# Optimization experiments

Hardware: AMD Instinct MI355X
Metric: run time of the kernel (lower is better)

## Reference

```python
import jax, jax.numpy as jnp
import numpy as np
from jax import lax

DN = ('NCHW', 'OIHW', 'NCHW')
BETA = 0.25


def _conv(x, w, b, stride, pad):
    y = lax.conv_general_dilated(x, w, (stride, stride), [(pad, pad), (pad, pad)],
                                 dimension_numbers=DN)
    return y + b[None, :, None, None]


def _convT(x, w, b, stride, pad, opad):
    # torch ConvTranspose2d(w: [in,out,kh,kw]) == dilated conv with flipped, transposed kernel
    k = w.shape[2]
    wf = jnp.transpose(w, (1, 0, 2, 3))[:, :, ::-1, ::-1]
    lo = k - 1 - pad
    hi = k - 1 - pad + opad
    y = lax.conv_general_dilated(x, wf, (1, 1), [(lo, hi), (lo, hi)],
                                 lhs_dilation=(stride, stride), dimension_numbers=DN)
    return y + b[None, :, None, None]


def setup_inputs() -> dict:
    key = jax.random.key(0)
    ks = jax.random.split(key, 16)
    s = 0.05
    inp = {
        'x': jax.random.normal(ks[0], (64, 3, 125, 125), jnp.float32),
        'enc_w1': jax.random.normal(ks[1], (32, 3, 3, 3), jnp.float32) * s,
        'enc_b1': jnp.zeros((32,), jnp.float32),
        'enc_w2': jax.random.normal(ks[2], (64, 32, 3, 3), jnp.float32) * s,
        'enc_b2': jnp.zeros((64,), jnp.float32),
        'enc_w3': jax.random.normal(ks[3], (64, 64, 1, 1), jnp.float32) * s,
        'enc_b3': jnp.zeros((64,), jnp.float32),
        'codebook': jax.random.normal(ks[4], (512, 64), jnp.float32),
        'dec_w1': jax.random.normal(ks[5], (64, 64, 3, 3), jnp.float32) * s,  # torch [in,out,kh,kw]
        'dec_b1': jnp.zeros((64,), jnp.float32),
        'dec_w2': jax.random.normal(ks[6], (64, 32, 3, 3), jnp.float32) * s,
        'dec_b2': jnp.zeros((32,), jnp.float32),
        'dec_w3': jax.random.normal(ks[7], (32, 3, 2, 2), jnp.float32) * s,
        'dec_b3': jnp.zeros((3,), jnp.float32),
    }
    return inp


def reference(x, enc_w1, enc_b1, enc_w2, enc_b2, enc_w3, enc_b3, codebook,
              dec_w1, dec_b1, dec_w2, dec_b2, dec_w3, dec_b3):
    # Encoder
    z = jax.nn.relu(_conv(x, enc_w1, enc_b1, 2, 1))
    z = jax.nn.relu(_conv(z, enc_w2, enc_b2, 2, 1))
    z = _conv(z, enc_w3, enc_b3, 1, 0)  # [B, D, h, w]

    # VQ (training mode)
    zp = jnp.transpose(z, (0, 2, 3, 1))  # [B, h, w, D]
    flat = zp.reshape(-1, zp.shape[-1])  # [N, D]
    d = (jnp.sum(flat * flat, axis=1, keepdims=True)
         + jnp.sum(codebook * codebook, axis=1)
         - 2.0 * flat @ codebook.T)  # [N, K]
    idx = jnp.argmin(d, axis=1)
    q = codebook[idx].reshape(zp.shape)

    q_latent_loss = jnp.mean((q - lax.stop_gradient(zp)) ** 2)
    e_latent_loss = jnp.mean((zp - lax.stop_gradient(q)) ** 2)
    e_q_loss = q_latent_loss + BETA * e_latent_loss

    q_st = zp + lax.stop_gradient(q - zp)  # straight-through
    e = jnp.transpose(q_st, (0, 3, 1, 2))

    # Decoder
    h = jax.nn.relu(_convT(e, dec_w1, dec_b1, 2, 1, 1))
    h = jax.nn.relu(_convT(h, dec_w2, dec_b2, 2, 1, 1))
    x_recon = _convT(h, dec_w3, dec_b3, 1, 2, 0)

    recon_loss = jnp.sum((x_recon - x) ** 2)
    loss_sum = e_q_loss + recon_loss
    return (loss_sum, e_q_loss, recon_loss, x_recon)
```

## Files before the change

kernel.cpp:

```cpp
#include <hip/hip_runtime.h>

#define DEV __device__ __forceinline__
typedef unsigned short u16;
typedef __bf16 bf16x8 __attribute__((ext_vector_type(8)));
typedef float f32x4 __attribute__((ext_vector_type(4)));

DEV u16 f2bf(float f) {
  unsigned u = __float_as_uint(f);
  u += 0x7FFF + ((u >> 16) & 1);
  return (u16)(u >> 16);
}


__global__ __launch_bounds__(256) void k_prep(
    const float* __restrict__ ew1, const float* __restrict__ ew2,
    const float* __restrict__ ew3, const float* __restrict__ dw1,
    const float* __restrict__ dw2, const float* __restrict__ dw3,
    const float* __restrict__ cb,
    float* __restrict__ wc1p, float* __restrict__ wc3p,
    u16* __restrict__ w3f, float* __restrict__ c2,
    u16* __restrict__ w2f, u16* __restrict__ wt1f, u16* __restrict__ wt2f,
    u16* __restrict__ cbf) {
  int i = blockIdx.x * 256 + threadIdx.x;
  if (i < 864) {
    int cl = i & 7; int t = i >> 3; int tap = t % 9; t /= 9; int ci = t % 3; int cog = t / 3;
    wc1p[i] = ew1[((cog * 8 + cl) * 3 + ci) * 9 + tap];
  } else if (i < 4960) {
    int j = i - 864; int cl = j & 7; int t = j >> 3; int ci = t & 63; int cog = t >> 6;
    wc3p[j] = ew3[(cog * 8 + cl) * 64 + ci];
  } else if (i < 9056) {
    int j = i - 4960;
    int jj = j & 7; int lane = (j >> 3) & 63; int tp = (j >> 9) & 3; int hl = j >> 11;
    int kh = tp >> 1, kw = tp & 1;
    int ci = ((lane >> 4) << 3) + jj; int co = lane & 15;
    float wv = (co < 3) ? dw3[((ci * 3 + co) * 2 + kh) * 2 + kw] : 0.f;
    u16 hi = f2bf(wv);
    if (hl == 0) w3f[j] = hi;
    else         w3f[j] = f2bf(wv - __uint_as_float((unsigned)hi << 16));
  } else if (i < 9568) {
    int k = i - 9056;
    const float4* c4 = (const float4*)(cb + (k << 6));
    float s = 0.f;
    #pragma unroll
    for (int q = 0; q < 16; ++q) { float4 v = c4[q]; s += v.x*v.x + v.y*v.y + v.z*v.z + v.w*v.w; }
    c2[k] = s;
  } else if (i < 28000) {
    int j = i - 9568;
    int jj = j & 7; int lane = (j >> 3) & 63; int nf = (j >> 9) & 3; int kt = j >> 11;
    int kh = kt / 3, kw = kt % 3;
    int ci = ((lane >> 4) << 3) + jj; int co = (nf << 4) + (lane & 15);
    w2f[j] = f2bf(ew2[((co * 32 + ci) * 3 + kh) * 3 + kw]);
  } else if (i < 64864) {
    int j = i - 28000;
    int jj = j & 7; int lane = (j >> 3) & 63; int nf = (j >> 9) & 3; int s = (j >> 11) & 1; int kt = j >> 12;
    int kh = kt / 3, kw = kt % 3;
    int ci = (s << 5) + ((lane >> 4) << 3) + jj; int co = (nf << 4) + (lane & 15);
    wt1f[j] = f2bf(dw1[((ci * 64 + co) * 3 + kh) * 3 + kw]);
  } else if (i < 83296) {
    int j = i - 64864;
    int jj = j & 7; int lane = (j >> 3) & 63; int nf = (j >> 9) & 1; int s = (j >> 10) & 1; int kt = j >> 11;
    int kh = kt / 3, kw = kt % 3;
    int ci = (s << 5) + ((lane >> 4) << 3) + jj; int co = (nf << 4) + (lane & 15);
    wt2f[j] = f2bf(dw2[((ci * 32 + co) * 3 + kh) * 3 + kw]);
  } else if (i < 148832) {
    int j = i - 83296;
    int jj = j & 7; int lane = (j >> 3) & 63; int nt = (j >> 9) & 31; int ks = (j >> 14) & 1; int hl = j >> 15;
    int ci = (ks << 5) + ((lane >> 4) << 3) + jj;
    int code = (nt << 4) + (lane & 15);
    float v = cb[(code << 6) + ci];
    u16 hi = f2bf(v);
    cbf[j] = hl ? f2bf(v - __uint_as_float((unsigned)hi << 16)) : hi;
  }
}

__global__ __launch_bounds__(256) void k_pad(
    const float* __restrict__ x, float* __restrict__ xp) {
  int idx = blockIdx.x * 256 + threadIdx.x;
  int c4 = idx & 31;
  int r  = (idx >> 5) % 129;
  int cbp = (idx >> 5) / 129;
  int ih = r - 1;
  float4 v = make_float4(0.f, 0.f, 0.f, 0.f);
  if ((unsigned)ih < 125u) {
    const float* rp = x + (cbp * 125 + ih) * 125;
    int iw0 = c4 * 4 - 1;
    if (iw0 >= 0)        v.x = rp[iw0];
    if (iw0 + 1 < 125)   v.y = rp[iw0 + 1];
    if (iw0 + 2 < 125)   v.z = rp[iw0 + 2];
    if (iw0 + 3 < 125)   v.w = rp[iw0 + 3];
  }
  *(float4*)(xp + (cbp * 129 + r) * 128 + c4 * 4) = v;
}

__global__ __launch_bounds__(256) void k_conv1(
    const float* __restrict__ xp, const float* __restrict__ wp,
    const float* __restrict__ bias, u16* __restrict__ z1t) {
  __shared__ u16 st[256 * 34];
  int t = threadIdx.x;
  int slab = blockIdx.x & 15, b = blockIdx.x >> 4;
  int tx = t & 15, ty = (t >> 4) & 3, cg = t >> 6;
  int oh = slab * 4 + ty;
  int co0 = cg * 8;
  const float* wcg = wp + cg * 216;
  float acc[8][4];
  #pragma unroll
  for (int c = 0; c < 8; ++c) {
    float bv = bias[co0 + c];
    #pragma unroll
    for (int s = 0; s < 4; ++s) acc[c][s] = bv;
  }
  #pragma unroll
  for (int ci = 0; ci < 3; ++ci) {
    #pragma unroll
    for (int kh = 0; kh < 3; ++kh) {
      const float* rp = xp + ((b * 3 + ci) * 129 + (2 * oh + kh)) * 128 + 8 * tx;
      float4 qa = *(const float4*)rp;
      float4 qb = *(const float4*)(rp + 4);
      float v8 = rp[8];
      float v[9] = {qa.x, qa.y, qa.z, qa.w, qb.x, qb.y, qb.z, qb.w, v8};
      #pragma unroll
      for (int kw = 0; kw < 3; ++kw) {
        const float* wq = wcg + (ci * 9 + kh * 3 + kw) * 8;
        float4 wa = *(const float4*)wq;
        float4 wb = *(const float4*)(wq + 4);
        float w8[8] = {wa.x, wa.y, wa.z, wa.w, wb.x, wb.y, wb.z, wb.w};
        #pragma unroll
        for (int s = 0; s < 4; ++s) {
          float in = v[2 * s + kw];
          #pragma unroll
          for (int c = 0; c < 8; ++c) acc[c][s] = fmaf(in, w8[c], acc[c][s]);
        }
      }
    }
  }
  #pragma unroll
  for (int s = 0; s < 4; ++s) {
    bool wok = (tx * 4 + s) < 63;
    unsigned p0 = 0, p1 = 0, p2 = 0, p3 = 0;
    if (wok) {
      p0 = f2bf(fmaxf(acc[0][s], 0.f)) | ((unsigned)f2bf(fmaxf(acc[1][s], 0.f)) << 16);
      p1 = f2bf(fmaxf(acc[2][s], 0.f)) | ((unsigned)f2bf(fmaxf(acc[3][s], 0.f)) << 16);
      p2 = f2bf(fmaxf(acc[4][s], 0.f)) | ((unsigned)f2bf(fmaxf(acc[5][s], 0.f)) << 16);
      p3 = f2bf(fmaxf(acc[6][s], 0.f)) | ((unsigned)f2bf(fmaxf(acc[7][s], 0.f)) << 16);
    }
    int lpix = tx * 16 + ty * 4 + s;
    *(uint4*)&st[lpix * 34 + co0] = make_uint4(p0, p1, p2, p3);
  }
  __syncthreads();
  {
    int p = t;
    int ow = (p >> 4) * 4 + (p & 3);
    int ohl = (p >> 2) & 3;
    int oho = slab * 4 + ohl;
    if (oho < 63) {
      const u16* lp = &st[p * 34];
      uint4 a0 = *(const uint4*)(lp);
      uint4 a1 = *(const uint4*)(lp + 8);
      uint4 a2 = *(const uint4*)(lp + 16);
      uint4 a3 = *(const uint4*)(lp + 24);
      uint4* gp = (uint4*)(z1t + ((b * 63 + oho) * 64 + ow) * 32);
      gp[0] = a0; gp[1] = a1; gp[2] = a2; gp[3] = a3;
    }
  }
}

__global__ __launch_bounds__(256) void k_conv2(
    const u16* __restrict__ z1t, const u16* __restrict__ wf,
    const float* __restrict__ bias, float* __restrict__ z2) {
  int t = threadIdx.x;
  int lane = t & 63, wv = t >> 6;
  int n = lane & 15, q = lane >> 4;
  int oh = blockIdx.x & 31, b = blockIdx.x >> 5;
  int xt = wv & 1, ch = wv >> 1;
  int xA = xt * 16 + n;
  f32x4 acc[2] = {{0,0,0,0},{0,0,0,0}};
  #pragma unroll
  for (int kh = 0; kh < 3; ++kh) {
    int ih = 2 * oh - 1 + kh;
    bool yok = (unsigned)ih < 63u;
    #pragma unroll
    for (int kw = 0; kw < 3; ++kw) {
      int iw = 2 * xA - 1 + kw;
      bool ok = yok && (iw >= 0);
      bf16x8 a = {};
      if (ok) a = *(const bf16x8*)(z1t + ((b * 63 + ih) * 64 + iw) * 32 + q * 8);
      int kt = kh * 3 + kw;
      const u16* wb = wf + ((kt << 2) + (ch << 1)) * 512 + lane * 8;
      bf16x8 b0 = *(const bf16x8*)wb;
      bf16x8 b1 = *(const bf16x8*)(wb + 512);
      acc[0] = __builtin_amdgcn_mfma_f32_16x16x32_bf16(a, b0, acc[0], 0, 0, 0);
      acc[1] = __builtin_amdgcn_mfma_f32_16x16x32_bf16(a, b1, acc[1], 0, 0, 0);
    }
  }
  #pragma unroll
  for (int j = 0; j < 2; ++j) {
    int co = ((ch << 1) + j) * 16 + n;
    float bv = bias[co];
    float4 rv = make_float4(fmaxf(acc[j][0] + bv, 0.f), fmaxf(acc[j][1] + bv, 0.f),
                            fmaxf(acc[j][2] + bv, 0.f), fmaxf(acc[j][3] + bv, 0.f));
    *(float4*)(z2 + ((b * 64 + co) * 32 + oh) * 32 + xt * 16 + q * 4) = rv;
  }
}

__global__ __launch_bounds__(256) void k_conv3(
    const float* __restrict__ in, const float* __restrict__ wp,
    const float* __restrict__ bias, float* __restrict__ z3,
    u16* __restrict__ z3h, u16* __restrict__ z3l) {
  __shared__ u16 lh[128 * 72];
  __shared__ u16 ll[128 * 72];
  int t = threadIdx.x;
  int pxg = blockIdx.x & 7; int b = blockIdx.x >> 3;
  int pxi = t & 31, cog = t >> 5;
  int px0 = pxg * 128 + pxi * 4;
  const float* wcg = wp + cog * 512;
  int co0 = cog * 8;
  float acc[8][4];
  #pragma unroll
  for (int c = 0; c < 8; ++c) {
    float bv = bias[co0 + c];
    #pragma unroll
    for (int s = 0; s < 4; ++s) acc[c][s] = bv;
  }
  const float* ip = in + (b << 16) + px0;
  for (int ci = 0; ci < 64; ++ci) {
    float4 v = *(const float4*)(ip + (ci << 10));
    float4 wa = *(const float4*)(wcg + ci * 8);
    float4 wb = *(const float4*)(wcg + ci * 8 + 4);
    float w8[8] = {wa.x, wa.y, wa.z, wa.w, wb.x, wb.y, wb.z, wb.w};
    #pragma unroll
    for (int c = 0; c < 8; ++c) {
      acc[c][0] = fmaf(v.x, w8[c], acc[c][0]);
      acc[c][1] = fmaf(v.y, w8[c], acc[c][1]);
      acc[c][2] = fmaf(v.z, w8[c], acc[c][2]);
      acc[c][3] = fmaf(v.w, w8[c], acc[c][3]);
    }
  }
  float* op = z3 + ((b << 6) + co0) * 1024 + px0;
  #pragma unroll
  for (int c = 0; c < 8; ++c)
    *(float4*)(op + (c << 10)) = make_float4(acc[c][0], acc[c][1], acc[c][2], acc[c][3]);
  #pragma unroll
  for (int s = 0; s < 4; ++s) {
    unsigned h[4], l[4];
    #pragma unroll
    for (int g = 0; g < 4; ++g) {
      float v0 = acc[2 * g][s], v1 = acc[2 * g + 1][s];
      u16 h0 = f2bf(v0), h1 = f2bf(v1);
      u16 l0 = f2bf(v0 - __uint_as_float((unsigned)h0 << 16));
      u16 l1 = f2bf(v1 - __uint_as_float((unsigned)h1 << 16));
      h[g] = h0 | ((unsigned)h1 << 16);
      l[g] = l0 | ((unsigned)l1 << 16);
    }
    int la = (pxi * 4 + s) * 72 + co0;
    *(uint4*)&lh[la] = make_uint4(h[0], h[1], h[2], h[3]);
    *(uint4*)&ll[la] = make_uint4(l[0], l[1], l[2], l[3]);
  }
  __syncthreads();
  {
    int p = t >> 1, half = t & 1;
    int la = p * 72 + half * 32;
    uint4 h0 = *(uint4*)&lh[la],      h1 = *(uint4*)&lh[la + 8];
    uint4 h2 = *(uint4*)&lh[la + 16], h3 = *(uint4*)&lh[la + 24];
    uint4 l0 = *(uint4*)&ll[la],      l1 = *(uint4*)&ll[la + 8];
    uint4 l2 = *(uint4*)&ll[la + 16], l3 = *(uint4*)&ll[la + 24];
    long gp = ((long)b * 1024 + pxg * 128 + p) * 64 + half * 32;
    uint4* oh = (uint4*)(z3h + gp);
    uint4* ol = (uint4*)(z3l + gp);
    oh[0] = h0; oh[1] = h1; oh[2] = h2; oh[3] = h3;
    ol[0] = l0; ol[1] = l1; ol[2] = l2; ol[3] = l3;
  }
}

__global__ __launch_bounds__(256) void k_vqp(
    const u16* __restrict__ z3h, const u16* __restrict__ z3l,
    const u16* __restrict__ cbf, const float* __restrict__ c2v,
    int* __restrict__ idxb) {
  int t = threadIdx.x;
  int lane = t & 63, wv = t >> 6;
  int n = lane & 15, q = lane >> 4;
  int p0 = blockIdx.x * 64;
  bf16x8 Ah[4][2], Al[4][2];
  #pragma unroll
  for (int mt = 0; mt < 4; ++mt) {
    const u16* ap = z3h + (p0 + mt * 16 + n) * 64 + q * 8;
    const u16* al = z3l + (p0 + mt * 16 + n) * 64 + q * 8;
    Ah[mt][0] = *(const bf16x8*)ap;  Ah[mt][1] = *(const bf16x8*)(ap + 32);
    Al[mt][0] = *(const bf16x8*)al;  Al[mt][1] = *(const bf16x8*)(al + 32);
  }
  float bs[4][4]; int bix[4][4];
  #pragma unroll
  for (int mt = 0; mt < 4; ++mt)
    #pragma unroll
    for (int r = 0; r < 4; ++r) { bs[mt][r] = 3.4e38f; bix[mt][r] = 0; }
  #pragma unroll
  for (int nt0 = 0; nt0 < 8; ++nt0) {
    int nt = wv * 8 + nt0;
    const u16* bp = cbf + lane * 8;
    bf16x8 Bh0 = *(const bf16x8*)(bp + (nt << 9));
    bf16x8 Bh1 = *(const bf16x8*)(bp + ((32 + nt) << 9));
    bf16x8 Bl0 = *(const bf16x8*)(bp + ((64 + nt) << 9));
    bf16x8 Bl1 = *(const bf16x8*)(bp + ((96 + nt) << 9));
    float c2 = c2v[(nt << 4) + n];
    #pragma unroll
    for (int mt = 0; mt < 4; ++mt) {
      f32x4 acc = {0.f, 0.f, 0.f, 0.f};
      acc = __builtin_amdgcn_mfma_f32_16x16x32_bf16(Ah[mt][0], Bh0, acc, 0, 0, 0);
      acc = __builtin_amdgcn_mfma_f32_16x16x32_bf16(Ah[mt][1], Bh1, acc, 0, 0, 0);
      acc = __builtin_amdgcn_mfma_f32_16x16x32_bf16(Al[mt][0], Bh0, acc, 0, 0, 0);
      acc = __builtin_amdgcn_mfma_f32_16x16x32_bf16(Al[mt][1], Bh1, acc, 0, 0, 0);
      acc = __builtin_amdgcn_mfma_f32_16x16x32_bf16(Ah[mt][0], Bl0, acc, 0, 0, 0);
      acc = __builtin_amdgcn_mfma_f32_16x16x32_bf16(Ah[mt][1], Bl1, acc, 0, 0, 0);
      int idx = (nt << 4) + n;
      #pragma unroll
      for (int r = 0; r < 4; ++r) {
        float sc = fmaf(-2.f, acc[r], c2);
        if (sc < bs[mt][r]) { bs[mt][r] = sc; bix[mt][r] = idx; }
      }
    }
  }
  #pragma unroll
  for (int off = 8; off > 0; off >>= 1) {
    #pragma unroll
    for (int mt = 0; mt < 4; ++mt)
      #pragma unroll
      for (int r = 0; r < 4; ++r) {
        float os = __shfl_xor(bs[mt][r], off, 16);
        int oi = __shfl_xor(bix[mt][r], off, 16);
        if (os < bs[mt][r] || (os == bs[mt][r] && oi < bix[mt][r])) {
          bs[mt][r] = os; bix[mt][r] = oi;
        }
      }
  }
  __shared__ float ls[4][64];
  __shared__ int   li[4][64];
  if (n == 0) {
    #pragma unroll
    for (int mt = 0; mt < 4; ++mt)
      #pragma unroll
      for (int r = 0; r < 4; ++r) {
        int px = mt * 16 + q * 4 + r;
        ls[wv][px] = bs[mt][r];
        li[wv][px] = bix[mt][r];
      }
  }
  __syncthreads();
  if (t < 64) {
    float best = ls[0][t]; int bi = li[0][t];
    #pragma unroll
    for (int w = 1; w < 4; ++w) {
      float s = ls[w][t]; int ii = li[w][t];
      if (s < best || (s == best && ii < bi)) { best = s; bi = ii; }
    }
    idxb[p0 + t] = bi;
  }
}

__global__ __launch_bounds__(256) void k_vqf(
    const float* __restrict__ z3, const float* __restrict__ cb,
    const int* __restrict__ idxb, u16* __restrict__ et,
    float* __restrict__ acc) {
  int n = blockIdx.x * 256 + threadIdx.x;
  int bi = idxb[n];
  int b = n >> 10, hw = n & 1023;
  const float* zp = z3 + (b << 16) + hw;
  uint2* ep = (uint2*)(et + (n << 6));
  const float4* cq = (const float4*)(cb + (bi << 6));
  float lsum = 0.f;
  #pragma unroll
  for (int i = 0; i < 16; ++i) {
    float4 c = cq[i];
    float zv, df;
    zv = zp[(4*i+0) << 10]; df = c.x - zv; lsum = fmaf(df, df, lsum);
    zv = zp[(4*i+1) << 10]; df = c.y - zv; lsum = fmaf(df, df, lsum);
    zv = zp[(4*i+2) << 10]; df = c.z - zv; lsum = fmaf(df, df, lsum);
    zv = zp[(4*i+3) << 10]; df = c.w - zv; lsum = fmaf(df, df, lsum);
    ep[i] = make_uint2(f2bf(c.x) | ((unsigned)f2bf(c.y) << 16),
                       f2bf(c.z) | ((unsigned)f2bf(c.w) << 16));
  }
  __shared__ float red[256];
  red[threadIdx.x] = lsum; __syncthreads();
  #pragma unroll
  for (int s = 128; s > 0; s >>= 1) {
    if (threadIdx.x < s) red[threadIdx.x] += red[threadIdx.x + s];
    __syncthreads();
  }
  if (threadIdx.x == 0) atomicAdd(acc + 0, red[0]);
}

__global__ __launch_bounds__(256) void k_convT1(
    const u16* __restrict__ et, const u16* __restrict__ wf,
    const float* __restrict__ bias, u16* __restrict__ h1t) {
  __shared__ u16 wl[36 * 512];
  __shared__ u16 st[4][64 * 34];
  int t = threadIdx.x;
  int lane = t & 63, wv = t >> 6;
  int yw = wv & 1, xt = wv >> 1;
  int cog = blockIdx.x & 1;
  int yg = (blockIdx.x >> 1) & 7;
  int b = blockIdx.x >> 4;
  {
    const uint4* gw = (const uint4*)wf;
    uint4* lw = (uint4*)wl;
    #pragma unroll
    for (int k = 0; k < 9; ++k) {
      int i = t + 256 * k;
      int slot = i >> 6, within = i & 63;
      int kt = slot >> 2, j = (slot >> 1) & 1, ks = slot & 1;
      int goff = (kt << 12) + (((ks << 2) + (cog << 1) + j) << 9);
      lw[i] = gw[(goff >> 3) + within];
    }
  }
  int n = lane & 15, q = lane >> 4;
  int m = xt * 16 + n;
  __syncthreads();
  for (int iter = 0; iter < 2; ++iter) {
    int y = yg * 4 + iter * 2 + yw;
    const u16* base0 = et + (((b * 32 + y) * 32) << 6) + q * 8;
    bf16x8 P00a, P00b, P01a = {}, P01b = {}, P10a = {}, P10b = {}, P11a = {}, P11b = {};
    { const u16* p = base0 + (m << 6); P00a = *(const bf16x8*)p; P00b = *(const bf16x8*)(p + 32); }
    if (m + 1 < 32) { const u16* p = base0 + ((m + 1) << 6); P01a = *(const bf16x8*)p; P01b = *(const bf16x8*)(p + 32); }
    if (y + 1 < 32) {
      const u16* base1 = base0 + (32 << 6);
      { const u16* p = base1 + (m << 6); P10a = *(const bf16x8*)p; P10b = *(const bf16x8*)(p + 32); }
      if (m + 1 < 32) { const u16* p = base1 + ((m + 1) << 6); P11a = *(const bf16x8*)p; P11b = *(const bf16x8*)(p + 32); }
    }
    f32x4 accE[2][2] = {};
    f32x4 accO[2][2] = {};
    #pragma unroll
    for (int kw = 0; kw < 3; ++kw) {
      int pwi = (kw == 1) ? 0 : 1;
      bf16x8 A0a = (kw == 0) ? P01a : P00a;
      bf16x8 A0b = (kw == 0) ? P01b : P00b;
      bf16x8 A1a = (kw == 0) ? P11a : P10a;
      bf16x8 A1b = (kw == 0) ? P11b : P10b;
      #pragma unroll
      for (int j = 0; j < 2; ++j) {
        const u16* wE  = wl + ((((3 + kw) << 2) + (j << 1)) << 9) + lane * 8;
        const u16* wO0 = wl + (((kw << 2) + (j << 1)) << 9) + lane * 8;
        const u16* wO2 = wl + ((((6 + kw) << 2) + (j << 1)) << 9) + lane * 8;
        bf16x8 bE0 = *(const bf16x8*)wE;
        bf16x8 bE1 = *(const bf16x8*)(wE + 512);
        accE[j][pwi] = __builtin_amdgcn_mfma_f32_16x16x32_bf16(A0a, bE0, accE[j][pwi], 0, 0, 0);
        accE[j][pwi] = __builtin_amdgcn_mfma_f32_16x16x32_bf16(A0b, bE1, accE[j][pwi], 0, 0, 0);
        bf16x8 bO00 = *(const bf16x8*)wO0;
        bf16x8 bO01 = *(const bf16x8*)(wO0 + 512);
        accO[j][pwi] = __builtin_amdgcn_mfma_f32_16x16x32_bf16(A1a, bO00, accO[j][pwi], 0, 0, 0);
        accO[j][pwi] = __builtin_amdgcn_mfma_f32_16x16x32_bf16(A1b, bO01, accO[j][pwi], 0, 0, 0);
        bf16x8 bO20 = *(const bf16x8*)wO2;
        bf16x8 bO21 = *(const bf16x8*)(wO2 + 512);
        accO[j][pwi] = __builtin_amdgcn_mfma_f32_16x16x32_bf16(A0a, bO20, accO[j][pwi], 0, 0, 0);
        accO[j][pwi] = __builtin_amdgcn_mfma_f32_16x16x32_bf16(A0b, bO21, accO[j][pwi], 0, 0, 0);
      }
    }
    #pragma unroll
    for (int j = 0; j < 2; ++j) {
      int col = j * 16 + n;
      float bv = bias[cog * 32 + col];
      #pragma unroll
      for (int pw = 0; pw < 2; ++pw)
        #pragma unroll
        for (int r = 0; r < 4; ++r) {
          int ow = 2 * (xt * 16 + q * 4 + r) + pw;
          st[yw * 2 + 0][ow * 34 + col] = f2bf(fmaxf(accE[j][pw][r] + bv, 0.f));
          st[yw * 2 + 1][ow * 34 + col] = f2bf(fmaxf(accO[j][pw][r] + bv, 0.f));
        }
    }
    __syncthreads();
    {
      int row = t >> 6, ow = t & 63;
      const u16* lp = &st[row][ow * 34];
      uint4* gp = (uint4*)(h1t + (((b * 64 + yg * 8 + iter * 4 + row) * 64 + ow) << 6) + cog * 32);
      gp[0] = *(const uint4*)(lp);
      gp[1] = *(const uint4*)(lp + 8);
      gp[2] = *(const uint4*)(lp + 16);
      gp[3] = *(const uint4*)(lp + 24);
    }
    __syncthreads();
  }
}

__global__ __launch_bounds__(256) void k_convT2(
    const u16* __restrict__ h1t, const u16* __restrict__ wf,
    const float* __restrict__ bias, u16* __restrict__ h2t) {
  __shared__ u16 wl[18432];
  __shared__ u16 st[2][128 * 34];
  int t = threadIdx.x;
  int lane = t & 63, xt = t >> 6;
  int n = lane & 15, q = lane >> 4;
  int yg = blockIdx.x & 15, b = blockIdx.x >> 4;
  {
    const uint4* gw = (const uint4*)wf;
    uint4* lw = (uint4*)wl;
    #pragma unroll
    for (int k = 0; k < 9; ++k) lw[t + 256 * k] = gw[t + 256 * k];
  }
  int m = xt * 16 + n;
  __syncthreads();
  for (int yp = 0; yp < 4; ++yp) {
    int y = yg * 4 + yp;
    const u16* base0 = h1t + (((b * 64 + y) * 64) << 6) + q * 8;
    bf16x8 P00a, P00b, P01a = {}, P01b = {}, P10a = {}, P10b = {}, P11a = {}, P11b = {};
    { const u16* p = base0 + (m << 6); P00a = *(const bf16x8*)p; P00b = *(const bf16x8*)(p + 32); }
    if (m + 1 < 64) { const u16* p = base0 + ((m + 1) << 6); P01a = *(const bf16x8*)p; P01b = *(const bf16x8*)(p + 32); }
    if (y + 1 < 64) {
      const u16* base1 = base0 + (64 << 6);
      { const u16* p = base1 + (m << 6); P10a = *(const bf16x8*)p; P10b = *(const bf16x8*)(p + 32); }
      if (m + 1 < 64) { const u16* p = base1 + ((m + 1) << 6); P11a = *(const bf16x8*)p; P11b = *(const bf16x8*)(p + 32); }
    }
    f32x4 accE[2][2] = {};
    f32x4 accO[2][2] = {};
    #pragma unroll
    for (int kw = 0; kw < 3; ++kw) {
      int pwi = (kw == 1) ? 0 : 1;
      bf16x8 A0a = (kw == 0) ? P01a : P00a;
      bf16x8 A0b = (kw == 0) ? P01b : P00b;
      bf16x8 A1a = (kw == 0) ? P11a : P10a;
      bf16x8 A1b = (kw == 0) ? P11b : P10b;
      const u16* wbE = wl + ((3 + kw) << 11) + lane * 8;
      const u16* wbO0 = wl + (kw << 11) + lane * 8;
      const u16* wbO2 = wl + ((6 + kw) << 11) + lane * 8;
      #pragma unroll
      for (int nf = 0; nf < 2; ++nf) {
        bf16x8 bE0 = *(const bf16x8*)(wbE + nf * 512);
        bf16x8 bE1 = *(const bf16x8*)(wbE + (2 + nf) * 512);
        accE[nf][pwi] = __builtin_amdgcn_mfma_f32_16x16x32_bf16(A0a, bE0, accE[nf][pwi], 0, 0, 0);
        accE[nf][pwi] = __builtin_amdgcn_mfma_f32_16x16x32_bf16(A0b, bE1, accE[nf][pwi], 0, 0, 0);
        bf16x8 bO00 = *(const bf16x8*)(wbO0 + nf * 512);
        bf16x8 bO01 = *(const bf16x8*)(wbO0 + (2 + nf) * 512);
        accO[nf][pwi] = __builtin_amdgcn_mfma_f32_16x16x32_bf16(A1a, bO00, accO[nf][pwi], 0, 0, 0);
        accO[nf][pwi] = __builtin_amdgcn_mfma_f32_16x16x32_bf16(A1b, bO01, accO[nf][pwi], 0, 0, 0);
        bf16x8 bO20 = *(const bf16x8*)(wbO2 + nf * 512);
        bf16x8 bO21 = *(const bf16x8*)(wbO2 + (2 + nf) * 512);
        accO[nf][pwi] = __builtin_amdgcn_mfma_f32_16x16x32_bf16(A0a, bO20, accO[nf][pwi], 0, 0, 0);
        accO[nf][pwi] = __builtin_amdgcn_mfma_f32_16x16x32_bf16(A0b, bO21, accO[nf][pwi], 0, 0, 0);
      }
    }
    #pragma unroll
    for (int nf = 0; nf < 2; ++nf) {
      int co = nf * 16 + n;
      float bv = bias[co];
      #pragma unroll
      for (int pw = 0; pw < 2; ++pw)
        #pragma unroll
        for (int r = 0; r < 4; ++r) {
          int ow = 2 * (xt * 16 + q * 4 + r) + pw;
          st[0][ow * 34 + co] = f2bf(fmaxf(accE[nf][pw][r] + bv, 0.f));
          st[1][ow * 34 + co] = f2bf(fmaxf(accO[nf][pw][r] + bv, 0.f));
        }
    }
    __syncthreads();
    {
      int ow = t >> 1, sg = t & 1;
      #pragma unroll
      for (int l = 0; l < 2; ++l) {
        const u16* lp = &st[l][ow * 34 + sg * 16];
        unsigned w0 = *(const unsigned*)(lp + 0), w1 = *(const unsigned*)(lp + 2);
        unsigned w2 = *(const unsigned*)(lp + 4), w3 = *(const unsigned*)(lp + 6);
        unsigned w4 = *(const unsigned*)(lp + 8), w5 = *(const unsigned*)(lp + 10);
        unsigned w6 = *(const unsigned*)(lp + 12), w7 = *(const unsigned*)(lp + 14);
        uint4* gp = (uint4*)(h2t + ((((b * 128 + yg * 8 + yp * 2 + l) * 128) + ow) << 5) + sg * 16);
        gp[0] = make_uint4(w0, w1, w2, w3);
        gp[1] = make_uint4(w4, w5, w6, w7);
      }
    }
    __syncthreads();
  }
}

__global__ __launch_bounds__(256) void k_convT3(
    const u16* __restrict__ h2t, const u16* __restrict__ w3f,
    const float* __restrict__ bias, const float* __restrict__ x,
    float* __restrict__ xr, float* __restrict__ psum) {
  int t = threadIdx.x;
  int lane = t & 63, wv = t >> 6;
  int n = lane & 15, q = lane >> 4;
  int oh = blockIdx.x % 125, b = blockIdx.x / 125;
  const u16* wbp = w3f + lane * 8;
  bf16x8 Bh0 = *(const bf16x8*)(wbp);
  bf16x8 Bh1 = *(const bf16x8*)(wbp + 512);
  bf16x8 Bh2 = *(const bf16x8*)(wbp + 1024);
  bf16x8 Bh3 = *(const bf16x8*)(wbp + 1536);
  bf16x8 Bl0 = *(const bf16x8*)(wbp + 2048);
  bf16x8 Bl1 = *(const bf16x8*)(wbp + 2560);
  bf16x8 Bl2 = *(const bf16x8*)(wbp + 3072);
  bf16x8 Bl3 = *(const bf16x8*)(wbp + 3584);
  const u16* row1 = h2t + (((long)b * 128 + (oh + 1)) << 7) * 32 + q * 8;
  const u16* row2 = row1 + 4096;
  float bv = (n < 3) ? bias[n] : 0.f;
  float lsum = 0.f;
  #pragma unroll
  for (int ti = 0; ti < 2; ++ti) {
    int tt = wv + ti * 4;
    int c1 = tt * 16 + n + 1;
    int c2 = c1 + 1;
    bf16x8 a11 = {}, a12 = {}, a21 = {}, a22 = {};
    if (c1 < 128) { a11 = *(const bf16x8*)(row1 + (c1 << 5));
                    a21 = *(const bf16x8*)(row2 + (c1 << 5)); }
    if (c2 < 128) { a12 = *(const bf16x8*)(row1 + (c2 << 5));
                    a22 = *(const bf16x8*)(row2 + (c2 << 5)); }
    f32x4 acc = {0.f, 0.f, 0.f, 0.f};
    acc = __builtin_amdgcn_mfma_f32_16x16x32_bf16(a11, Bh3, acc, 0, 0, 0);
    acc = __builtin_amdgcn_mfma_f32_16x16x32_bf16(a12, Bh2, acc, 0, 0, 0);
    acc = __builtin_amdgcn_mfma_f32_16x16x32_bf16(a21, Bh1, acc, 0, 0, 0);
    acc = __builtin_amdgcn_mfma_f32_16x16x32_bf16(a22, Bh0, acc, 0, 0, 0);
    acc = __builtin_amdgcn_mfma_f32_16x16x32_bf16(a11, Bl3, acc, 0, 0, 0);
    acc = __builtin_amdgcn_mfma_f32_16x16x32_bf16(a12, Bl2, acc, 0, 0, 0);
    acc = __builtin_amdgcn_mfma_f32_16x16x32_bf16(a21, Bl1, acc, 0, 0, 0);
    acc = __builtin_amdgcn_mfma_f32_16x16x32_bf16(a22, Bl0, acc, 0, 0, 0);
    if (n < 3) {
      int ow0 = tt * 16 + q * 4;
      int o = b * 46875 + n * 15625 + oh * 125 + ow0;
      if (ow0 + 3 < 125) {
        float4 v = make_float4(acc[0] + bv, acc[1] + bv, acc[2] + bv, acc[3] + bv);
        float4 xv = *(const float4*)(x + o);
        *(float4*)(xr + o) = v;
        float d0 = v.x - xv.x, d1 = v.y - xv.y, d2 = v.z - xv.z, d3 = v.w - xv.w;
        lsum += d0 * d0 + d1 * d1 + d2 * d2 + d3 * d3;
      } else {
        #pragma unroll
        for (int r = 0; r < 4; ++r) {
          if (ow0 + r < 125) {
            float v = acc[r] + bv;
            xr[o + r] = v;
            float d = v - x[o + r];
            lsum = fmaf(d, d, lsum);
          }
        }
      }
    }
  }
  __shared__ float red[256];
  red[t] = lsum; __syncthreads();
  #pragma unroll
  for (int s = 128; s > 0; s >>= 1) {
    if (t < s) red[t] += red[t + s];
    __syncthreads();
  }
  if (t == 0) psum[blockIdx.x] = red[0];
}

__global__ __launch_bounds__(256) void k_fin(
    const float* __restrict__ acc, const float* __restrict__ psum,
    float* __restrict__ out) {
  int t = threadIdx.x;
  float s = 0.f;
  for (int i = t; i < 8000; i += 256) s += psum[i];
  __shared__ float red[256];
  red[t] = s; __syncthreads();
  #pragma unroll
  for (int k = 128; k > 0; k >>= 1) {
    if (t < k) red[t] += red[t + k];
    __syncthreads();
  }
  if (t == 0) {
    float eq  = 1.25f * acc[0] / 4194304.0f;
    float rec = red[0];
    out[0] = eq + rec;
    out[1] = eq;
    out[2] = rec;
  }
}

extern "C" void kernel_launch(void* const* d_in, const int* in_sizes, int n_in,
                              void* d_out, int out_size, void* d_ws, size_t ws_size,
                              hipStream_t stream) {
  (void)in_sizes; (void)n_in; (void)out_size; (void)ws_size;
  const float* x   = (const float*)d_in[0];
  const float* ew1 = (const float*)d_in[1];
  const float* eb1 = (const float*)d_in[2];
  const float* ew2 = (const float*)d_in[3];
  const float* eb2 = (const float*)d_in[4];
  const float* ew3 = (const float*)d_in[5];
  const float* eb3 = (const float*)d_in[6];
  const float* cb  = (const float*)d_in[7];
  const float* dw1 = (const float*)d_in[8];
  const float* db1 = (const float*)d_in[9];
  const float* dw2 = (const float*)d_in[10];
  const float* db2 = (const float*)d_in[11];
  const float* dw3 = (const float*)d_in[12];
  const float* db3 = (const float*)d_in[13];
  float* out = (float*)d_out;
  char*  ws  = (char*)d_ws;

  float*  acc  = (float*)(ws + 0);
  float*  c2   = (float*)(ws + 256);
  float*  wc1p = (float*)(ws + 4096);
  float*  wc3p = (float*)(ws + 8192);
  u16*    w3f  = (u16*)  (ws + 24576);
  u16*    w2f  = (u16*)  (ws + 36864);
  u16*    wt1f = (u16*)  (ws + 73728);
  u16*    wt2f = (u16*)  (ws + 147456);
  float*  psum = (float*)(ws + 184320);
  u16*    cbf  = (u16*)  (ws + 262144);
  u16*    z1t  = (u16*)  (ws + 1048576);
  float*  z2   = (float*)(ws + 18874368);
  float*  z3   = (float*)(ws + 35651584);
  int*    idxb = (int*)  (ws + 52428800);
  u16*    et   = (u16*)  (ws + 54525952);
  u16*    h1t  = (u16*)  (ws + 1048576);
  u16*    h2t  = (u16*)  (ws + 67108864);
  u16*    z3h  = (u16*)  (ws + 134217728);
  u16*    z3l  = (u16*)  (ws + 142606336);
  float*  xp   = (float*)(ws + 150994944);

  hipMemsetAsync(acc, 0, 64, stream);
  k_prep  <<<582,  256, 0, stream>>>(ew1, ew2, ew3, dw1, dw2, dw3, cb,
                                     wc1p, wc3p, w3f, c2, w2f, wt1f, wt2f, cbf);
  k_pad   <<<3096, 256, 0, stream>>>(x, xp);
  k_conv1 <<<1024, 256, 0, stream>>>(xp, wc1p, eb1, z1t);
  k_conv2 <<<2048, 256, 0, stream>>>(z1t, w2f, eb2, z2);
  k_conv3 <<<512,  256, 0, stream>>>(z2, wc3p, eb3, z3, z3h, z3l);
  k_vqp   <<<1024, 256, 0, stream>>>(z3h, z3l, cbf, c2, idxb);
  k_vqf   <<<256,  256, 0, stream>>>(z3, cb, idxb, et, acc);
  k_convT1<<<1024, 256, 0, stream>>>(et, wt1f, db1, h1t);
  k_convT2<<<1024, 256, 0, stream>>>(h1t, wt2f, db2, h2t);
  k_convT3<<<8000, 256, 0, stream>>>(h2t, w3f, db3, x, out + 3, psum);
  k_fin   <<<1,    256, 0, stream>>>(acc, psum, out);
}
```

Baseline: 292.9 us.

## Remap block indices across XCDs and give convT3 blocks four output rows

```diff
diff --git a/kernel.cpp b/kernel.cpp
--- a/kernel.cpp
+++ b/kernel.cpp
@@ -170,7 +170,9 @@
   int t = threadIdx.x;
   int lane = t & 63, wv = t >> 6;
   int n = lane & 15, q = lane >> 4;
-  int oh = blockIdx.x & 31, b = blockIdx.x >> 5;
+  int raw = blockIdx.x;
+  int wg = ((raw & 7) << 8) + (raw >> 3);
+  int oh = wg & 31, b = wg >> 5;
   int xt = wv & 1, ch = wv >> 1;
   int xA = xt * 16 + n;
   f32x4 acc[2] = {{0,0,0,0},{0,0,0,0}};
@@ -395,9 +397,11 @@
   int t = threadIdx.x;
   int lane = t & 63, wv = t >> 6;
   int yw = wv & 1, xt = wv >> 1;
-  int cog = blockIdx.x & 1;
-  int yg = (blockIdx.x >> 1) & 7;
-  int b = blockIdx.x >> 4;
+  int raw = blockIdx.x;
+  int wg = ((raw & 7) << 7) + (raw >> 3);
+  int cog = wg & 1;
+  int yg = (wg >> 1) & 7;
+  int b = wg >> 4;
   {
     const uint4* gw = (const uint4*)wf;
     uint4* lw = (uint4*)wl;
@@ -487,7 +491,9 @@
   int t = threadIdx.x;
   int lane = t & 63, xt = t >> 6;
   int n = lane & 15, q = lane >> 4;
-  int yg = blockIdx.x & 15, b = blockIdx.x >> 4;
+  int raw = blockIdx.x;
+  int wg = ((raw & 7) << 7) + (raw >> 3);
+  int yg = wg & 15, b = wg >> 4;
   {
     const uint4* gw = (const uint4*)wf;
     uint4* lw = (uint4*)wl;
@@ -574,7 +580,10 @@
   int t = threadIdx.x;
   int lane = t & 63, wv = t >> 6;
   int n = lane & 15, q = lane >> 4;
-  int oh = blockIdx.x % 125, b = blockIdx.x / 125;
+  int raw = blockIdx.x;
+  int wg = ((raw & 7) << 8) + (raw >> 3);
+  int rg = wg & 31, b = wg >> 5;
+  int oh0 = rg * 4;
   const u16* wbp = w3f + lane * 8;
   bf16x8 Bh0 = *(const bf16x8*)(wbp);
   bf16x8 Bh1 = *(const bf16x8*)(wbp + 512);
@@ -584,46 +593,51 @@
   bf16x8 Bl1 = *(const bf16x8*)(wbp + 2560);
   bf16x8 Bl2 = *(const bf16x8*)(wbp + 3072);
   bf16x8 Bl3 = *(const bf16x8*)(wbp + 3584);
-  const u16* row1 = h2t + (((long)b * 128 + (oh + 1)) << 7) * 32 + q * 8;
-  const u16* row2 = row1 + 4096;
   float bv = (n < 3) ? bias[n] : 0.f;
   float lsum = 0.f;
-  #pragma unroll
-  for (int ti = 0; ti < 2; ++ti) {
-    int tt = wv + ti * 4;
-    int c1 = tt * 16 + n + 1;
-    int c2 = c1 + 1;
-    bf16x8 a11 = {}, a12 = {}, a21 = {}, a22 = {};
-    if (c1 < 128) { a11 = *(const bf16x8*)(row1 + (c1 << 5));
-                    a21 = *(const bf16x8*)(row2 + (c1 << 5)); }
-    if (c2 < 128) { a12 = *(const bf16x8*)(row1 + (c2 << 5));
-                    a22 = *(const bf16x8*)(row2 + (c2 << 5)); }
-    f32x4 acc = {0.f, 0.f, 0.f, 0.f};
-    acc = __builtin_amdgcn_mfma_f32_16x16x32_bf16(a11, Bh3, acc, 0, 0, 0);
-    acc = __builtin_amdgcn_mfma_f32_16x16x32_bf16(a12, Bh2, acc, 0, 0, 0);
-    acc = __builtin_amdgcn_mfma_f32_16x16x32_bf16(a21, Bh1, acc, 0, 0, 0);
-    acc = __builtin_amdgcn_mfma_f32_16x16x32_bf16(a22, Bh0, acc, 0, 0, 0);
-    acc = __builtin_amdgcn_mfma_f32_16x16x32_bf16(a11, Bl3, acc, 0, 0, 0);
-    acc = __builtin_amdgcn_mfma_f32_16x16x32_bf16(a12, Bl2, acc, 0, 0, 0);
-    acc = __builtin_amdgcn_mfma_f32_16x16x32_bf16(a21, Bl1, acc, 0, 0, 0);
-    acc = __builtin_amdgcn_mfma_f32_16x16x32_bf16(a22, Bl0, acc, 0, 0, 0);
-    if (n < 3) {
-      int ow0 = tt * 16 + q * 4;
-      int o = b * 46875 + n * 15625 + oh * 125 + ow0;
-      if (ow0 + 3 < 125) {
-        float4 v = make_float4(acc[0] + bv, acc[1] + bv, acc[2] + bv, acc[3] + bv);
-        float4 xv = *(const float4*)(x + o);
-        *(float4*)(xr + o) = v;
-        float d0 = v.x - xv.x, d1 = v.y - xv.y, d2 = v.z - xv.z, d3 = v.w - xv.w;
-        lsum += d0 * d0 + d1 * d1 + d2 * d2 + d3 * d3;
-      } else {
-        #pragma unroll
-        for (int r = 0; r < 4; ++r) {
-          if (ow0 + r < 125) {
-            float v = acc[r] + bv;
-            xr[o + r] = v;
-            float d = v - x[o + r];
-            lsum = fmaf(d, d, lsum);
+  for (int r4 = 0; r4 < 4; ++r4) {
+    int oh = oh0 + r4;
+    if (oh < 125) {
+      const u16* row1 = h2t + (((long)b * 128 + (oh + 1)) << 12) + q * 8;
+      const u16* row2 = row1 + 4096;
+      #pragma unroll
+      for (int ti = 0; ti < 2; ++ti) {
+        int tt = wv + ti * 4;
+        int c1 = tt * 16 + n + 1;
+        int c2 = c1 + 1;
+        bf16x8 a11 = {}, a12 = {}, a21 = {}, a22 = {};
+        if (c1 < 128) { a11 = *(const bf16x8*)(row1 + (c1 << 5));
+                        a21 = *(const bf16x8*)(row2 + (c1 << 5)); }
+        if (c2 < 128) { a12 = *(const bf16x8*)(row1 + (c2 << 5));
+                        a22 = *(const bf16x8*)(row2 + (c2 << 5)); }
+        f32x4 acc = {0.f, 0.f, 0.f, 0.f};
+        acc = __builtin_amdgcn_mfma_f32_16x16x32_bf16(a11, Bh3, acc, 0, 0, 0);
+        acc = __builtin_amdgcn_mfma_f32_16x16x32_bf16(a12, Bh2, acc, 0, 0, 0);
+        acc = __builtin_amdgcn_mfma_f32_16x16x32_bf16(a21, Bh1, acc, 0, 0, 0);
+        acc = __builtin_amdgcn_mfma_f32_16x16x32_bf16(a22, Bh0, acc, 0, 0, 0);
+        acc = __builtin_amdgcn_mfma_f32_16x16x32_bf16(a11, Bl3, acc, 0, 0, 0);
+        acc = __builtin_amdgcn_mfma_f32_16x16x32_bf16(a12, Bl2, acc, 0, 0, 0);
+        acc = __builtin_amdgcn_mfma_f32_16x16x32_bf16(a21, Bl1, acc, 0, 0, 0);
+        acc = __builtin_amdgcn_mfma_f32_16x16x32_bf16(a22, Bl0, acc, 0, 0, 0);
+        if (n < 3) {
+          int ow0 = tt * 16 + q * 4;
+          int o = b * 46875 + n * 15625 + oh * 125 + ow0;
+          if (ow0 + 3 < 125) {
+            float4 v = make_float4(acc[0] + bv, acc[1] + bv, acc[2] + bv, acc[3] + bv);
+            float4 xv = *(const float4*)(x + o);
+            *(float4*)(xr + o) = v;
+            float d0 = v.x - xv.x, d1 = v.y - xv.y, d2 = v.z - xv.z, d3 = v.w - xv.w;
+            lsum += d0 * d0 + d1 * d1 + d2 * d2 + d3 * d3;
+          } else {
+            #pragma unroll
+            for (int r = 0; r < 4; ++r) {
+              if (ow0 + r < 125) {
+                float v = acc[r] + bv;
+                xr[o + r] = v;
+                float d = v - x[o + r];
+                lsum = fmaf(d, d, lsum);
+              }
+            }
           }
         }
       }
@@ -636,7 +650,7 @@
     if (t < s) red[t] += red[t + s];
     __syncthreads();
   }
-  if (t == 0) psum[blockIdx.x] = red[0];
+  if (t == 0) psum[raw] = red[0];
 }
 
 __global__ __launch_bounds__(256) void k_fin(
@@ -644,7 +658,7 @@
     float* __restrict__ out) {
   int t = threadIdx.x;
   float s = 0.f;
-  for (int i = t; i < 8000; i += 256) s += psum[i];
+  for (int i = t; i < 2048; i += 256) s += psum[i];
   __shared__ float red[256];
   red[t] = s; __syncthreads();
   #pragma unroll
@@ -714,6 +728,6 @@
   k_vqf   <<<256,  256, 0, stream>>>(z3, cb, idxb, et, acc);
   k_convT1<<<1024, 256, 0, stream>>>(et, wt1f, db1, h1t);
   k_convT2<<<1024, 256, 0, stream>>>(h1t, wt2f, db2, h2t);
-  k_convT3<<<8000, 256, 0, stream>>>(h2t, w3f, db3, x, out + 3, psum);
+  k_convT3<<<2048, 256, 0, stream>>>(h2t, w3f, db3, x, out + 3, psum);
   k_fin   <<<1,    256, 0, stream>>>(acc, psum, out);
 }
```

Result: no change. 289.5 us (-1.2%).
